# Kernel tuning notes

Measured on AMD Instinct MI355X. Metric: run time of the kernel, lower is better.

The kernel has to match this reference:

```python
import jax, jax.numpy as jnp
import numpy as np

C = 512
NUM_HEADS = 8
HEAD_DIM = C // NUM_HEADS
GROUPS = 32
EPS = 1e-5


def setup_inputs() -> dict:
    key = jax.random.key(0)
    ks = jax.random.split(key, 7)
    N, H, W = 16, 32, 32
    x = jax.random.normal(ks[0], (N, C, H, W), dtype=jnp.float32)
    norm_w = jax.random.normal(ks[1], (C,), dtype=jnp.float32) * 0.02 + 1.0
    norm_b = jax.random.normal(ks[2], (C,), dtype=jnp.float32) * 0.02
    qkv_w = jax.random.normal(ks[3], (3 * C, C), dtype=jnp.float32) * (1.0 / np.sqrt(C))
    qkv_b = jax.random.normal(ks[4], (3 * C,), dtype=jnp.float32) * 0.02
    proj_w = jax.random.normal(ks[5], (C, C), dtype=jnp.float32) * (1.0 / np.sqrt(C))
    proj_b = jax.random.normal(ks[6], (C,), dtype=jnp.float32) * 0.02
    return {"x": x, "norm_w": norm_w, "norm_b": norm_b, "qkv_w": qkv_w,
            "qkv_b": qkv_b, "proj_w": proj_w, "proj_b": proj_b}


def _group_norm(x, w, b):
    N, Cc, H, W = x.shape
    xg = x.reshape(N, GROUPS, Cc // GROUPS, H, W)
    mean = xg.mean(axis=(2, 3, 4), keepdims=True)
    var = xg.var(axis=(2, 3, 4), keepdims=True)
    xg = (xg - mean) * jax.lax.rsqrt(var + EPS)
    return xg.reshape(N, Cc, H, W) * w[None, :, None, None] + b[None, :, None, None]


def reference(x, norm_w, norm_b, qkv_w, qkv_b, proj_w, proj_b):
    N, Cc, H, W = x.shape
    S = H * W
    h = _group_norm(x, norm_w, norm_b)
    # 1x1 conv == per-pixel linear over channels
    qkv = jnp.einsum('nchw,oc->nohw', h, qkv_w) + qkv_b[None, :, None, None]
    q, k, v = jnp.split(qkv, 3, axis=1)  # each [N, C, H, W]
    # [N, heads, head_dim, S]
    q = q.reshape(N, NUM_HEADS, HEAD_DIM, S)
    k = k.reshape(N, NUM_HEADS, HEAD_DIM, S)
    v = v.reshape(N, NUM_HEADS, HEAD_DIM, S)
    scale = HEAD_DIM ** -0.5
    attn = jnp.einsum('nhds,nhdt->nhst', q, k) * scale  # [N,heads,S,S]
    attn = jax.nn.softmax(attn, axis=-1)
    out = jnp.einsum('nhst,nhdt->nhds', attn, v)  # [N,heads,head_dim,S]
    out = out.reshape(N, Cc, H, W)
    out = jnp.einsum('nchw,oc->nohw', out, proj_w) + proj_b[None, :, None, None]
    return out + x
```

## Files before the change

### kernel.cpp

```cpp
#include <hip/hip_runtime.h>
#include <cstdint>
#include <cstddef>

typedef unsigned short u16;
typedef __attribute__((ext_vector_type(8))) short bf16x8;
typedef __attribute__((ext_vector_type(4))) short bf16x4;
typedef __attribute__((ext_vector_type(4))) float f32x4;
typedef __attribute__((ext_vector_type(16))) float f32x16;
typedef __attribute__((ext_vector_type(4))) unsigned short u16x4;

#define NB 16
#define CD 512
#define SD 1024
#define NH 8
#define HD 64

#define QSCL 0.18033688011112042f

__device__ __forceinline__ u16 f2bf(float f) {
    unsigned u = __float_as_uint(f);
    u += 0x7FFF + ((u >> 16) & 1);
    return (u16)(u >> 16);
}
__device__ __forceinline__ unsigned cvt_pk(float lo, float hi) {
    unsigned r;
    asm("v_cvt_pk_bf16_f32 %0, %1, %2" : "=v"(r) : "v"(lo), "v"(hi));
    return r;
}
__device__ __forceinline__ float exp2v(float x) {
    float r;
    asm("v_exp_f32 %0, %1" : "=v"(r) : "v"(x));
    return r;
}
__device__ __forceinline__ void gload16(const void* g, void* l) {
    __builtin_amdgcn_global_load_lds(
        (const __attribute__((address_space(1))) void*)g,
        (__attribute__((address_space(3))) void*)l, 16, 0, 0);
}

__global__ __launch_bounds__(256) void cvt2_kernel(
    const float* __restrict__ s0, u16* __restrict__ d0,
    const float* __restrict__ s1, u16* __restrict__ d1)
{
    const int bid = blockIdx.x;
    const float* s;
    u16* d;
    int i;
    if (bid < 768) { s = s0; d = d0; i = (bid * 256 + threadIdx.x) * 4; }
    else           { s = s1; d = d1; i = ((bid - 768) * 256 + threadIdx.x) * 4; }
    float4 v = *reinterpret_cast<const float4*>(s + i);
    u16x4 o = { f2bf(v.x), f2bf(v.y), f2bf(v.z), f2bf(v.w) };
    *reinterpret_cast<u16x4*>(d + i) = o;
}

__global__ __launch_bounds__(256) void gn_kernel(
    const float* __restrict__ x, const float* __restrict__ w,
    const float* __restrict__ b, u16* __restrict__ h)
{
    const int n = blockIdx.x >> 5, g = blockIdx.x & 31;
    const size_t base = ((size_t)n * CD + g * 16) * SD;
    const float4* xp = reinterpret_cast<const float4*>(x + base);

    float4 vals[16];
    float sum = 0.f, ss = 0.f;
#pragma unroll
    for (int i = 0; i < 16; ++i) {
        float4 v = xp[threadIdx.x + (i << 8)];
        vals[i] = v;
        sum += v.x + v.y + v.z + v.w;
        ss  += v.x*v.x + v.y*v.y + v.z*v.z + v.w*v.w;
    }
#pragma unroll
    for (int off = 32; off > 0; off >>= 1) {
        sum += __shfl_down(sum, off);
        ss  += __shfl_down(ss,  off);
    }
    __shared__ float rs[4], rq[4];
    const int wid = threadIdx.x >> 6, lane = threadIdx.x & 63;
    if (lane == 0) { rs[wid] = sum; rq[wid] = ss; }
    __syncthreads();
    const float tsum = rs[0] + rs[1] + rs[2] + rs[3];
    const float tss  = rq[0] + rq[1] + rq[2] + rq[3];
    const float mean = tsum * (1.0f / 16384.0f);
    const float var  = tss * (1.0f / 16384.0f) - mean * mean;
    const float inv  = rsqrtf(var + 1e-5f);

    u16* hp = h + ((size_t)n * SD + 4 * threadIdx.x) * CD + g * 16;
#pragma unroll
    for (int i = 0; i < 16; ++i) {
        const float A  = inv * w[g * 16 + i];
        const float Bc = b[g * 16 + i] - mean * A;
        float4 v = vals[i];
        hp[i]          = f2bf(v.x * A + Bc);
        hp[CD + i]     = f2bf(v.y * A + Bc);
        hp[2 * CD + i] = f2bf(v.z * A + Bc);
        hp[3 * CD + i] = f2bf(v.w * A + Bc);
    }
}

template<int MODE>
__global__ __launch_bounds__(256, 4) void mfma_gemm(
    const u16* __restrict__ Wb, const u16* __restrict__ act,
    const float* __restrict__ bias, const float* __restrict__ resid,
    void* __restrict__ outp, u16* __restrict__ vtout, int M)
{
    const int nb = blockIdx.z, m0 = blockIdx.y * 128, s0 = blockIdx.x * 128;
    __shared__ u16 Al[128 * 64];
    __shared__ u16 Bl[128 * 64];
    const int tid = threadIdx.x, wv = tid >> 6, ln = tid & 63;
    const int wm = wv >> 1, wn = wv & 1, lr = ln & 15, lg = ln >> 4;

    const f32x4 zero = {0.f, 0.f, 0.f, 0.f};
    f32x4 acc[4][4];
#pragma unroll
    for (int i = 0; i < 4; ++i)
#pragma unroll
        for (int j = 0; j < 4; ++j) acc[i][j] = zero;

    const u16* Ab = Wb + (size_t)m0 * CD;
    const u16* Bb = act + ((size_t)nb * SD + s0) * CD;

    for (int k0 = 0; k0 < CD; k0 += 64) {
        __syncthreads();
#pragma unroll
        for (int r = 0; r < 4; ++r) {
            const int gi = (r * 4 + wv) * 64 + ln;
            const int row = gi >> 3, gc = gi & 7;
            const int sg = ((gc ^ (row & 7)) * 8);
            gload16(Ab + (size_t)row * CD + k0 + sg, Al + gi * 8);
            gload16(Bb + (size_t)row * CD + k0 + sg, Bl + gi * 8);
        }
        __syncthreads();

#pragma unroll
        for (int kc = 0; kc < 2; ++kc) {
            bf16x8 af[4], bfr[4];
#pragma unroll
            for (int mi = 0; mi < 4; ++mi) {
                const int row = wm * 64 + mi * 16 + lr;
                af[mi] = *reinterpret_cast<const bf16x8*>(
                    Al + row * 64 + (((kc * 4 + lg) ^ (row & 7)) * 8));
            }
#pragma unroll
            for (int nj = 0; nj < 4; ++nj) {
                const int row = wn * 64 + nj * 16 + lr;
                bfr[nj] = *reinterpret_cast<const bf16x8*>(
                    Bl + row * 64 + (((kc * 4 + lg) ^ (row & 7)) * 8));
            }
#pragma unroll
            for (int mi = 0; mi < 4; ++mi)
#pragma unroll
                for (int nj = 0; nj < 4; ++nj) {
                    if (MODE == 0)
                        acc[mi][nj] = __builtin_amdgcn_mfma_f32_16x16x32_bf16(
                            af[mi], bfr[nj], acc[mi][nj], 0, 0, 0);
                    else
                        acc[mi][nj] = __builtin_amdgcn_mfma_f32_16x16x32_bf16(
                            bfr[mi], af[nj], acc[mi][nj], 0, 0, 0);
                }
        }
    }

    if (MODE == 0) {
        if (m0 < 1024) {
            u16* o = (u16*)outp;
            const float sc = (m0 < 512) ? QSCL : 1.0f;
#pragma unroll
            for (int mi = 0; mi < 4; ++mi) {
                const int mb = m0 + wm * 64 + mi * 16 + lg * 4;
#pragma unroll
                for (int nj = 0; nj < 4; ++nj) {
                    const int s = s0 + wn * 64 + nj * 16 + lr;
                    u16x4 pack;
#pragma unroll
                    for (int r = 0; r < 4; ++r)
                        pack[r] = f2bf((acc[mi][nj][r] + bias[mb + r]) * sc);
                    *reinterpret_cast<u16x4*>(o + ((size_t)nb * SD + s) * 1024 + mb) = pack;
                }
            }
        } else {
            const int sswap = (lg >= 2) ? 4 : 0;
            const int sbase = (s0 + wn * 64 + lr) ^ sswap;
            const int mb = m0 - 1024 + wm * 64 + lg * 4;
            u16* vb = vtout + ((size_t)nb * 512 + mb) * SD + sbase;
            const float* bp = bias + m0 + wm * 64 + lg * 4;
#pragma unroll
            for (int mi = 0; mi < 4; ++mi)
#pragma unroll
                for (int r = 0; r < 4; ++r) {
                    const float bi = bp[mi * 16 + r];
#pragma unroll
                    for (int nj = 0; nj < 4; ++nj)
                        vb[(size_t)(mi * 16 + r) * SD + nj * 16] =
                            f2bf(acc[mi][nj][r] + bi);
                }
        }
    } else {
        float* o = (float*)outp;
#pragma unroll
        for (int i = 0; i < 4; ++i)
#pragma unroll
            for (int j = 0; j < 4; ++j) {
                const int m = m0 + wm * 64 + j * 16 + lr;
                const int s = s0 + wn * 64 + i * 16 + lg * 4;
                const float bi = bias[m];
                const size_t idx = ((size_t)nb * M + m) * SD + s;
                float4 r4 = *reinterpret_cast<const float4*>(resid + idx);
                float4 v;
                v.x = acc[i][j][0] + bi + r4.x;
                v.y = acc[i][j][1] + bi + r4.y;
                v.z = acc[i][j][2] + bi + r4.z;
                v.w = acc[i][j][3] + bi + r4.w;
                *reinterpret_cast<float4*>(o + idx) = v;
            }
    }
}

__global__ __launch_bounds__(512) void attn_mfma(
    const u16* __restrict__ qk, const u16* __restrict__ vt, u16* __restrict__ ao)
{
    const int nh = blockIdx.y, n = nh >> 3, hh = nh & 7;
    const int q0 = blockIdx.x << 8;
    const int tid = threadIdx.x, wv = tid >> 6, ln = tid & 63;
    const int lq = ln & 31, hi = ln >> 5;

    __shared__ u16 Kl[2][64 * 64];
    __shared__ u16 Vl[2][64 * 64];

    const u16* Qb = qk + (size_t)n * SD * 1024 + hh * HD;
    const u16* Kb = Qb + 512;
    const u16* Vb = vt + ((size_t)n * 512 + hh * HD) * SD;

    bf16x8 qf[4];
    {
        const u16* qp = Qb + (size_t)(q0 + wv * 32 + lq) * 1024 + hi * 8;
#pragma unroll
        for (int ks = 0; ks < 4; ++ks)
            qf[ks] = *reinterpret_cast<const bf16x8*>(qp + ks * 16);
    }

    f32x16 of0 = {}, of1 = {};
    float mrun = -INFINITY, lrun = 0.f;

    const int srow = tid >> 3, sgc = tid & 7;
    const int ssw = (sgc ^ (srow & 7)) * 8;
    const u16* Ksrc = Kb + (size_t)srow * 1024 + ssw;
    const u16* Vsrc = Vb + (size_t)srow * SD + ssw;

    gload16(Ksrc, &Kl[0][tid * 8]);
    gload16(Vsrc, &Vl[0][tid * 8]);
    __syncthreads();

    const int hkey = (hi ^ ((lq >> 3) & 1)) * 4;
    int cur = 0;
    for (int tt = 0; tt < 16; ++tt) {
        if (tt < 15) {
            const int t1 = (tt + 1) << 6;
            gload16(Ksrc + (size_t)t1 * 1024, &Kl[cur ^ 1][tid * 8]);
            gload16(Vsrc + t1, &Vl[cur ^ 1][tid * 8]);
        }
        f32x16 st0 = {}, st1 = {};
        const u16* Kc = &Kl[cur][0];
        __builtin_amdgcn_s_setprio(1);
#pragma unroll
        for (int ks = 0; ks < 4; ++ks) {
            const int g = (((ks * 2 + hi) ^ (lq & 7)) * 8);
            bf16x8 k0 = *reinterpret_cast<const bf16x8*>(Kc + lq * 64 + g);
            bf16x8 k1 = *reinterpret_cast<const bf16x8*>(Kc + (32 + lq) * 64 + g);
            st0 = __builtin_amdgcn_mfma_f32_32x32x16_bf16(k0, qf[ks], st0, 0, 0, 0);
            st1 = __builtin_amdgcn_mfma_f32_32x32x16_bf16(k1, qf[ks], st1, 0, 0, 0);
        }
        __builtin_amdgcn_s_setprio(0);
        float tm[8];
#pragma unroll
        for (int i = 0; i < 8; ++i)
            tm[i] = fmaxf(fmaxf(st0[i], st0[i + 8]), fmaxf(st1[i], st1[i + 8]));
        float mx = fmaxf(fmaxf(fmaxf(tm[0], tm[1]), fmaxf(tm[2], tm[3])),
                         fmaxf(fmaxf(tm[4], tm[5]), fmaxf(tm[6], tm[7])));
        mx = fmaxf(mx, __shfl_xor(mx, 32));
        if (!__all(mx - mrun <= 8.0f)) {
            const float mn = fmaxf(mrun, mx);
            const float al = exp2v(mrun - mn);
            mrun = mn;
            lrun *= al;
#pragma unroll
            for (int r = 0; r < 16; ++r) { of0[r] *= al; of1[r] *= al; }
        }
        float sa = 0.f, sb = 0.f, sc = 0.f, sd = 0.f;
#pragma unroll
        for (int r = 0; r < 16; r += 4) {
            st0[r]     = exp2v(st0[r]     - mrun); sa += st0[r];
            st0[r + 1] = exp2v(st0[r + 1] - mrun); sb += st0[r + 1];
            st0[r + 2] = exp2v(st0[r + 2] - mrun); sc += st0[r + 2];
            st0[r + 3] = exp2v(st0[r + 3] - mrun); sd += st0[r + 3];
        }
#pragma unroll
        for (int r = 0; r < 16; r += 4) {
            st1[r]     = exp2v(st1[r]     - mrun); sa += st1[r];
            st1[r + 1] = exp2v(st1[r + 1] - mrun); sb += st1[r + 1];
            st1[r + 2] = exp2v(st1[r + 2] - mrun); sc += st1[r + 2];
            st1[r + 3] = exp2v(st1[r + 3] - mrun); sd += st1[r + 3];
        }
        float ps = (sa + sb) + (sc + sd);
        ps += __shfl_xor(ps, 32);
        lrun += ps;

        const u16* Vc = &Vl[cur][0];
        __builtin_amdgcn_s_setprio(1);
#pragma unroll
        for (int ks = 0; ks < 4; ++ks) {
            union { unsigned w[4]; bf16x8 v; } pf;
            const int rb = (ks & 1) * 8;
            if (ks < 2) {
                pf.w[0] = cvt_pk(st0[rb + 0], st0[rb + 1]);
                pf.w[1] = cvt_pk(st0[rb + 2], st0[rb + 3]);
                pf.w[2] = cvt_pk(st0[rb + 4], st0[rb + 5]);
                pf.w[3] = cvt_pk(st0[rb + 6], st0[rb + 7]);
            } else {
                pf.w[0] = cvt_pk(st1[rb + 0], st1[rb + 1]);
                pf.w[1] = cvt_pk(st1[rb + 2], st1[rb + 3]);
                pf.w[2] = cvt_pk(st1[rb + 4], st1[rb + 5]);
                pf.w[3] = cvt_pk(st1[rb + 6], st1[rb + 7]);
            }
            const int e0 = ((2 * ks) ^ (lq & 7)) * 8 + hkey;
            const int e1 = ((2 * ks + 1) ^ (lq & 7)) * 8 + hkey;
            union { bf16x4 h[2]; bf16x8 v; } vf0, vf1;
            vf0.h[0] = *reinterpret_cast<const bf16x4*>(Vc + lq * 64 + e0);
            vf0.h[1] = *reinterpret_cast<const bf16x4*>(Vc + lq * 64 + e1);
            vf1.h[0] = *reinterpret_cast<const bf16x4*>(Vc + (32 + lq) * 64 + e0);
            vf1.h[1] = *reinterpret_cast<const bf16x4*>(Vc + (32 + lq) * 64 + e1);
            of0 = __builtin_amdgcn_mfma_f32_32x32x16_bf16(vf0.v, pf.v, of0, 0, 0, 0);
            of1 = __builtin_amdgcn_mfma_f32_32x32x16_bf16(vf1.v, pf.v, of1, 0, 0, 0);
        }
        __builtin_amdgcn_s_setprio(0);
        __syncthreads();
        cur ^= 1;
    }

    const float inv = 1.0f / lrun;
    u16* op = ao + ((size_t)n * SD + q0 + wv * 32 + lq) * CD + hh * HD;
#pragma unroll
    for (int g = 0; g < 4; ++g) {
        u16x4 o0, o1;
#pragma unroll
        for (int e = 0; e < 4; ++e) {
            o0[e] = f2bf(of0[g * 4 + e] * inv);
            o1[e] = f2bf(of1[g * 4 + e] * inv);
        }
        const int d0 = g * 8 + hi * 4;
        *reinterpret_cast<u16x4*>(op + d0) = o0;
        *reinterpret_cast<u16x4*>(op + 32 + d0) = o1;
    }
}

extern "C" void kernel_launch(void* const* d_in, const int* in_sizes, int n_in,
                              void* d_out, int out_size, void* d_ws, size_t ws_size,
                              hipStream_t stream)
{
    const float* x      = (const float*)d_in[0];
    const float* norm_w = (const float*)d_in[1];
    const float* norm_b = (const float*)d_in[2];
    const float* qkv_w  = (const float*)d_in[3];
    const float* qkv_b  = (const float*)d_in[4];
    const float* proj_w = (const float*)d_in[5];
    const float* proj_b = (const float*)d_in[6];

    u16* h   = (u16*)d_ws;
    u16* qkb = h + (size_t)NB * SD * CD;
    u16* vtb = qkb + (size_t)NB * SD * 1024;
    u16* ao  = vtb + (size_t)NB * 512 * SD;
    u16* wq  = ao + (size_t)NB * SD * CD;
    u16* wp  = wq + (size_t)1536 * CD;

    hipLaunchKernelGGL(cvt2_kernel, dim3(1024), dim3(256), 0, stream,
                       qkv_w, wq, proj_w, wp);
    hipLaunchKernelGGL(gn_kernel, dim3(NB * 32), dim3(256), 0, stream, x, norm_w, norm_b, h);
    hipLaunchKernelGGL((mfma_gemm<0>), dim3(8, 12, NB), dim3(256), 0, stream,
                       wq, h, qkv_b, (const float*)nullptr, (void*)qkb, vtb, 1536);
    hipLaunchKernelGGL(attn_mfma, dim3(SD / 256, NB * NH), dim3(512), 0, stream,
                       qkb, vtb, ao);
    hipLaunchKernelGGL((mfma_gemm<1>), dim3(8, 4, NB), dim3(256), 0, stream,
                       wp, ao, proj_b, x, (void*)d_out, (u16*)nullptr, 512);
}
```

Before: 217.7 us.

## Load two KV tiles per barrier in attention and vectorize groupnorm stores

The attention loop now stages two 64-key K/V tiles per double-buffer set, so it runs 8 iterations with one barrier each instead of 16, roughly halving barrier and synchronisation overhead. The per-tile body is split into inline helpers. Shared memory doubles to 64KB per block, which may lower occupancy. Separately, the groupnorm kernel precomputes scale and shift and writes bf16 outputs as 16-byte vectors instead of scalar 2-byte stores.

```diff
diff --git a/kernel.cpp b/kernel.cpp
--- a/kernel.cpp
+++ b/kernel.cpp
@@ -8,6 +8,7 @@
 typedef __attribute__((ext_vector_type(4))) float f32x4;
 typedef __attribute__((ext_vector_type(16))) float f32x16;
 typedef __attribute__((ext_vector_type(4))) unsigned short u16x4;
+typedef __attribute__((ext_vector_type(8))) unsigned short u16x8;
 
 #define NB 16
 #define CD 512
@@ -85,16 +86,30 @@
     const float var  = tss * (1.0f / 16384.0f) - mean * mean;
     const float inv  = rsqrtf(var + 1e-5f);
 
+    float Af[16], Bf[16];
+#pragma unroll
+    for (int i = 0; i < 16; ++i) {
+        Af[i] = inv * w[g * 16 + i];
+        Bf[i] = b[g * 16 + i] - mean * Af[i];
+    }
     u16* hp = h + ((size_t)n * SD + 4 * threadIdx.x) * CD + g * 16;
 #pragma unroll
-    for (int i = 0; i < 16; ++i) {
-        const float A  = inv * w[g * 16 + i];
-        const float Bc = b[g * 16 + i] - mean * A;
-        float4 v = vals[i];
-        hp[i]          = f2bf(v.x * A + Bc);
-        hp[CD + i]     = f2bf(v.y * A + Bc);
-        hp[2 * CD + i] = f2bf(v.z * A + Bc);
-        hp[3 * CD + i] = f2bf(v.w * A + Bc);
+    for (int j = 0; j < 4; ++j) {
+        u16x8 o0, o1;
+#pragma unroll
+        for (int c = 0; c < 8; ++c) {
+            const float v = (j == 0) ? vals[c].x : (j == 1) ? vals[c].y
+                          : (j == 2) ? vals[c].z : vals[c].w;
+            o0[c] = f2bf(v * Af[c] + Bf[c]);
+        }
+#pragma unroll
+        for (int c = 0; c < 8; ++c) {
+            const float v = (j == 0) ? vals[c + 8].x : (j == 1) ? vals[c + 8].y
+                          : (j == 2) ? vals[c + 8].z : vals[c + 8].w;
+            o1[c] = f2bf(v * Af[c + 8] + Bf[c + 8]);
+        }
+        *reinterpret_cast<u16x8*>(hp + j * CD)     = o0;
+        *reinterpret_cast<u16x8*>(hp + j * CD + 8) = o1;
     }
 }
 
@@ -216,6 +231,101 @@
     }
 }
 
+__device__ __forceinline__ void qkt_tile(
+    const u16* Kc, const bf16x8 qf[4], int lq, int hi,
+    f32x16& st0, f32x16& st1)
+{
+    const f32x16 z = {};
+    st0 = z; st1 = z;
+    __builtin_amdgcn_s_setprio(1);
+#pragma unroll
+    for (int ks = 0; ks < 4; ++ks) {
+        const int g = (((ks * 2 + hi) ^ (lq & 7)) * 8);
+        bf16x8 k0 = *reinterpret_cast<const bf16x8*>(Kc + lq * 64 + g);
+        bf16x8 k1 = *reinterpret_cast<const bf16x8*>(Kc + (32 + lq) * 64 + g);
+        st0 = __builtin_amdgcn_mfma_f32_32x32x16_bf16(k0, qf[ks], st0, 0, 0, 0);
+        st1 = __builtin_amdgcn_mfma_f32_32x32x16_bf16(k1, qf[ks], st1, 0, 0, 0);
+    }
+    __builtin_amdgcn_s_setprio(0);
+}
+
+__device__ __forceinline__ void softmax_tile(
+    f32x16& st0, f32x16& st1, float& mrun, float& lrun,
+    f32x16& of0, f32x16& of1, unsigned* pfw)
+{
+    float tm[8];
+#pragma unroll
+    for (int i = 0; i < 8; ++i)
+        tm[i] = fmaxf(fmaxf(st0[i], st0[i + 8]), fmaxf(st1[i], st1[i + 8]));
+    float mx = fmaxf(fmaxf(fmaxf(tm[0], tm[1]), fmaxf(tm[2], tm[3])),
+                     fmaxf(fmaxf(tm[4], tm[5]), fmaxf(tm[6], tm[7])));
+    mx = fmaxf(mx, __shfl_xor(mx, 32));
+    if (!__all(mx - mrun <= 8.0f)) {
+        const float mn = fmaxf(mrun, mx);
+        const float al = exp2v(mrun - mn);
+        mrun = mn;
+        lrun *= al;
+#pragma unroll
+        for (int r = 0; r < 16; ++r) { of0[r] *= al; of1[r] *= al; }
+    }
+    float sa = 0.f, sb = 0.f, sc = 0.f, sd = 0.f;
+#pragma unroll
+    for (int r = 0; r < 16; r += 4) {
+        st0[r]     = exp2v(st0[r]     - mrun); sa += st0[r];
+        st0[r + 1] = exp2v(st0[r + 1] - mrun); sb += st0[r + 1];
+        st0[r + 2] = exp2v(st0[r + 2] - mrun); sc += st0[r + 2];
+        st0[r + 3] = exp2v(st0[r + 3] - mrun); sd += st0[r + 3];
+    }
+#pragma unroll
+    for (int r = 0; r < 16; r += 4) {
+        st1[r]     = exp2v(st1[r]     - mrun); sa += st1[r];
+        st1[r + 1] = exp2v(st1[r + 1] - mrun); sb += st1[r + 1];
+        st1[r + 2] = exp2v(st1[r + 2] - mrun); sc += st1[r + 2];
+        st1[r + 3] = exp2v(st1[r + 3] - mrun); sd += st1[r + 3];
+    }
+    float ps = (sa + sb) + (sc + sd);
+    ps += __shfl_xor(ps, 32);
+    lrun += ps;
+#pragma unroll
+    for (int ks = 0; ks < 4; ++ks) {
+        const int rb = (ks & 1) * 8;
+        if (ks < 2) {
+            pfw[ks * 4 + 0] = cvt_pk(st0[rb + 0], st0[rb + 1]);
+            pfw[ks * 4 + 1] = cvt_pk(st0[rb + 2], st0[rb + 3]);
+            pfw[ks * 4 + 2] = cvt_pk(st0[rb + 4], st0[rb + 5]);
+            pfw[ks * 4 + 3] = cvt_pk(st0[rb + 6], st0[rb + 7]);
+        } else {
+            pfw[ks * 4 + 0] = cvt_pk(st1[rb + 0], st1[rb + 1]);
+            pfw[ks * 4 + 1] = cvt_pk(st1[rb + 2], st1[rb + 3]);
+            pfw[ks * 4 + 2] = cvt_pk(st1[rb + 4], st1[rb + 5]);
+            pfw[ks * 4 + 3] = cvt_pk(st1[rb + 6], st1[rb + 7]);
+        }
+    }
+}
+
+__device__ __forceinline__ void pv_tile(
+    const u16* Vc, const unsigned* pfw, int lq, int hkey,
+    f32x16& of0, f32x16& of1)
+{
+    __builtin_amdgcn_s_setprio(1);
+#pragma unroll
+    for (int ks = 0; ks < 4; ++ks) {
+        union { unsigned w[4]; bf16x8 v; } pf;
+        pf.w[0] = pfw[ks * 4 + 0]; pf.w[1] = pfw[ks * 4 + 1];
+        pf.w[2] = pfw[ks * 4 + 2]; pf.w[3] = pfw[ks * 4 + 3];
+        const int e0 = ((2 * ks) ^ (lq & 7)) * 8 + hkey;
+        const int e1 = ((2 * ks + 1) ^ (lq & 7)) * 8 + hkey;
+        union { bf16x4 h[2]; bf16x8 v; } vf0, vf1;
+        vf0.h[0] = *reinterpret_cast<const bf16x4*>(Vc + lq * 64 + e0);
+        vf0.h[1] = *reinterpret_cast<const bf16x4*>(Vc + lq * 64 + e1);
+        vf1.h[0] = *reinterpret_cast<const bf16x4*>(Vc + (32 + lq) * 64 + e0);
+        vf1.h[1] = *reinterpret_cast<const bf16x4*>(Vc + (32 + lq) * 64 + e1);
+        of0 = __builtin_amdgcn_mfma_f32_32x32x16_bf16(vf0.v, pf.v, of0, 0, 0, 0);
+        of1 = __builtin_amdgcn_mfma_f32_32x32x16_bf16(vf1.v, pf.v, of1, 0, 0, 0);
+    }
+    __builtin_amdgcn_s_setprio(0);
+}
+
 __global__ __launch_bounds__(512) void attn_mfma(
     const u16* __restrict__ qk, const u16* __restrict__ vt, u16* __restrict__ ao)
 {
@@ -224,8 +334,8 @@
     const int tid = threadIdx.x, wv = tid >> 6, ln = tid & 63;
     const int lq = ln & 31, hi = ln >> 5;
 
-    __shared__ u16 Kl[2][64 * 64];
-    __shared__ u16 Vl[2][64 * 64];
+    __shared__ u16 Kl[2][2][64 * 64];
+    __shared__ u16 Vl[2][2][64 * 64];
 
     const u16* Qb = qk + (size_t)n * SD * 1024 + hh * HD;
     const u16* Kb = Qb + 512;
@@ -247,94 +357,33 @@
     const u16* Ksrc = Kb + (size_t)srow * 1024 + ssw;
     const u16* Vsrc = Vb + (size_t)srow * SD + ssw;
 
-    gload16(Ksrc, &Kl[0][tid * 8]);
-    gload16(Vsrc, &Vl[0][tid * 8]);
+    gload16(Ksrc,                     &Kl[0][0][tid * 8]);
+    gload16(Ksrc + (size_t)64 * 1024, &Kl[0][1][tid * 8]);
+    gload16(Vsrc,                     &Vl[0][0][tid * 8]);
+    gload16(Vsrc + 64,                &Vl[0][1][tid * 8]);
     __syncthreads();
 
     const int hkey = (hi ^ ((lq >> 3) & 1)) * 4;
-    int cur = 0;
-    for (int tt = 0; tt < 16; ++tt) {
-        if (tt < 15) {
-            const int t1 = (tt + 1) << 6;
-            gload16(Ksrc + (size_t)t1 * 1024, &Kl[cur ^ 1][tid * 8]);
-            gload16(Vsrc + t1, &Vl[cur ^ 1][tid * 8]);
-        }
-        f32x16 st0 = {}, st1 = {};
-        const u16* Kc = &Kl[cur][0];
-        __builtin_amdgcn_s_setprio(1);
-#pragma unroll
-        for (int ks = 0; ks < 4; ++ks) {
-            const int g = (((ks * 2 + hi) ^ (lq & 7)) * 8);
-            bf16x8 k0 = *reinterpret_cast<const bf16x8*>(Kc + lq * 64 + g);
-            bf16x8 k1 = *reinterpret_cast<const bf16x8*>(Kc + (32 + lq) * 64 + g);
-            st0 = __builtin_amdgcn_mfma_f32_32x32x16_bf16(k0, qf[ks], st0, 0, 0, 0);
-            st1 = __builtin_amdgcn_mfma_f32_32x32x16_bf16(k1, qf[ks], st1, 0, 0, 0);
-        }
-        __builtin_amdgcn_s_setprio(0);
-        float tm[8];
-#pragma unroll
-        for (int i = 0; i < 8; ++i)
-            tm[i] = fmaxf(fmaxf(st0[i], st0[i + 8]), fmaxf(st1[i], st1[i + 8]));
-        float mx = fmaxf(fmaxf(fmaxf(tm[0], tm[1]), fmaxf(tm[2], tm[3])),
-                         fmaxf(fmaxf(tm[4], tm[5]), fmaxf(tm[6], tm[7])));
-        mx = fmaxf(mx, __shfl_xor(mx, 32));
-        if (!__all(mx - mrun <= 8.0f)) {
-            const float mn = fmaxf(mrun, mx);
-            const float al = exp2v(mrun - mn);
-            mrun = mn;
-            lrun *= al;
-#pragma unroll
-            for (int r = 0; r < 16; ++r) { of0[r] *= al; of1[r] *= al; }
-        }
-        float sa = 0.f, sb = 0.f, sc = 0.f, sd = 0.f;
-#pragma unroll
-        for (int r = 0; r < 16; r += 4) {
-            st0[r]     = exp2v(st0[r]     - mrun); sa += st0[r];
-            st0[r + 1] = exp2v(st0[r + 1] - mrun); sb += st0[r + 1];
-            st0[r + 2] = exp2v(st0[r + 2] - mrun); sc += st0[r + 2];
-            st0[r + 3] = exp2v(st0[r + 3] - mrun); sd += st0[r + 3];
-        }
-#pragma unroll
-        for (int r = 0; r < 16; r += 4) {
-            st1[r]     = exp2v(st1[r]     - mrun); sa += st1[r];
-            st1[r + 1] = exp2v(st1[r + 1] - mrun); sb += st1[r + 1];
-            st1[r + 2] = exp2v(st1[r + 2] - mrun); sc += st1[r + 2];
-            st1[r + 3] = exp2v(st1[r + 3] - mrun); sd += st1[r + 3];
-        }
-        float ps = (sa + sb) + (sc + sd);
-        ps += __shfl_xor(ps, 32);
-        lrun += ps;
-
-        const u16* Vc = &Vl[cur][0];
-        __builtin_amdgcn_s_setprio(1);
-#pragma unroll
-        for (int ks = 0; ks < 4; ++ks) {
-            union { unsigned w[4]; bf16x8 v; } pf;
-            const int rb = (ks & 1) * 8;
-            if (ks < 2) {
-                pf.w[0] = cvt_pk(st0[rb + 0], st0[rb + 1]);
-                pf.w[1] = cvt_pk(st0[rb + 2], st0[rb + 3]);
-                pf.w[2] = cvt_pk(st0[rb + 4], st0[rb + 5]);
-                pf.w[3] = cvt_pk(st0[rb + 6], st0[rb + 7]);
-            } else {
-                pf.w[0] = cvt_pk(st1[rb + 0], st1[rb + 1]);
-                pf.w[1] = cvt_pk(st1[rb + 2], st1[rb + 3]);
-                pf.w[2] = cvt_pk(st1[rb + 4], st1[rb + 5]);
-                pf.w[3] = cvt_pk(st1[rb + 6], st1[rb + 7]);
-            }
-            const int e0 = ((2 * ks) ^ (lq & 7)) * 8 + hkey;
-            const int e1 = ((2 * ks + 1) ^ (lq & 7)) * 8 + hkey;
-            union { bf16x4 h[2]; bf16x8 v; } vf0, vf1;
-            vf0.h[0] = *reinterpret_cast<const bf16x4*>(Vc + lq * 64 + e0);
-            vf0.h[1] = *reinterpret_cast<const bf16x4*>(Vc + lq * 64 + e1);
-            vf1.h[0] = *reinterpret_cast<const bf16x4*>(Vc + (32 + lq) * 64 + e0);
-            vf1.h[1] = *reinterpret_cast<const bf16x4*>(Vc + (32 + lq) * 64 + e1);
-            of0 = __builtin_amdgcn_mfma_f32_32x32x16_bf16(vf0.v, pf.v, of0, 0, 0, 0);
-            of1 = __builtin_amdgcn_mfma_f32_32x32x16_bf16(vf1.v, pf.v, of1, 0, 0, 0);
-        }
-        __builtin_amdgcn_s_setprio(0);
+
+    for (int p = 0; p < 8; ++p) {
+        const int set = p & 1;
+        if (p < 7) {
+            const size_t tk = (size_t)(2 * p + 2) * 64 * 1024;
+            const int tv = (2 * p + 2) * 64;
+            gload16(Ksrc + tk,                     &Kl[set ^ 1][0][tid * 8]);
+            gload16(Ksrc + tk + (size_t)64 * 1024, &Kl[set ^ 1][1][tid * 8]);
+            gload16(Vsrc + tv,                     &Vl[set ^ 1][0][tid * 8]);
+            gload16(Vsrc + tv + 64,                &Vl[set ^ 1][1][tid * 8]);
+        }
+        f32x16 st0, st1;
+        unsigned pfw[16];
+        qkt_tile(&Kl[set][0][0], qf, lq, hi, st0, st1);
+        softmax_tile(st0, st1, mrun, lrun, of0, of1, pfw);
+        pv_tile(&Vl[set][0][0], pfw, lq, hkey, of0, of1);
+        qkt_tile(&Kl[set][1][0], qf, lq, hi, st0, st1);
+        softmax_tile(st0, st1, mrun, lrun, of0, of1, pfw);
+        pv_tile(&Vl[set][1][0], pfw, lq, hkey, of0, of1);
         __syncthreads();
-        cur ^= 1;
     }
 
     const float inv = 1.0f / lrun;
```

Result: slower. 225.8 us (+3.7%).
